# Kernel tuning notes

Measured on AMD Instinct MI355X. Metric: run time of the kernel, lower is better.

## Reference

```python
import jax, jax.numpy as jnp
import numpy as np

C = 256
NUM_HEADS = 4
GROUPS = 32  # max(1, 256//8), divides 256
EPS = 1e-5


def setup_inputs() -> dict:
    key = jax.random.key(0)
    ks = jax.random.split(key, 7)
    B, H, W = 4, 64, 64
    s = 0.02
    return {
        "x": jax.random.normal(ks[0], (B, C, H, W), dtype=jnp.float32),
        "norm_gamma": jnp.ones((C,), jnp.float32),
        "norm_beta": jnp.zeros((C,), jnp.float32),
        "qkv_w": jax.random.normal(ks[1], (3 * C, C), jnp.float32) * s,  # 1x1 conv kernel squeezed
        "qkv_b": jax.random.normal(ks[2], (3 * C,), jnp.float32) * s,
        "proj_w": jax.random.normal(ks[3], (C, C), jnp.float32) * s,
        "proj_b": jax.random.normal(ks[4], (C,), jnp.float32) * s,
    }


def reference(x, norm_gamma, norm_beta, qkv_w, qkv_b, proj_w, proj_b):
    B, Cc, H, W = x.shape
    hd = Cc // NUM_HEADS
    scale = hd ** -0.5

    # GroupNorm over (channels-per-group, H, W)
    xg = x.reshape(B, GROUPS, Cc // GROUPS, H, W)
    mu = xg.mean(axis=(2, 3, 4), keepdims=True)
    var = xg.var(axis=(2, 3, 4), keepdims=True)
    h = ((xg - mu) * jax.lax.rsqrt(var + EPS)).reshape(B, Cc, H, W)
    h = h * norm_gamma[:, None, None] + norm_beta[:, None, None]

    # 1x1 conv QKV: [B,3C,H,W]
    qkv = jnp.einsum('bchw,oc->bohw', h, qkv_w) + qkv_b[:, None, None]
    q, k, v = jnp.split(qkv, 3, axis=1)

    def heads(t):  # [B,C,H,W] -> [B,nh,HW,hd]
        return t.reshape(B, NUM_HEADS, hd, H * W).transpose(0, 1, 3, 2)

    q, k, v = heads(q), heads(k), heads(v)
    attn = jnp.einsum('bhnd,bhmd->bhnm', q, k) * scale  # [B,nh,HW,HW]
    attn = jax.nn.softmax(attn, axis=-1)
    out = jnp.einsum('bhnm,bhmd->bhnd', attn, v)  # [B,nh,HW,hd]
    out = out.transpose(0, 1, 3, 2).reshape(B, Cc, H, W)

    out = jnp.einsum('bchw,oc->bohw', out, proj_w) + proj_b[:, None, None]
    return x + out
```

## Files before the change

kernel.cpp:

```cpp
#include <hip/hip_runtime.h>
#include <hip/hip_bf16.h>
#include <stdint.h>

typedef unsigned short u16;
typedef __attribute__((ext_vector_type(8))) short bf16x8;
typedef __attribute__((ext_vector_type(4))) float f32x4;
typedef __attribute__((ext_vector_type(16))) float f32x16;

#define HW 4096
#define CC 256
#define QSCALE 0.18033688011112042f

__device__ __forceinline__ u16 f2bf(float f) {
    union { float f; uint32_t i; } v; v.f = f;
    uint32_t x = v.i;
    return (u16)((x + 0x7fffu + ((x >> 16) & 1u)) >> 16);
}

__device__ __forceinline__ float fast_exp2(float x) {
#if __has_builtin(__builtin_amdgcn_exp2f)
    return __builtin_amdgcn_exp2f(x);
#else
    return exp2f(x);
#endif
}

__device__ __forceinline__ unsigned cvt_pk_bf16(float lo, float hi) {
    unsigned r;
    asm("v_cvt_pk_bf16_f32 %0, %1, %2" : "=v"(r) : "v"(lo), "v"(hi));
    return r;
}

__device__ __forceinline__ void plane_swap(unsigned& a, unsigned& b) {
#if __has_builtin(__builtin_amdgcn_permlane32_swap)
    auto r = __builtin_amdgcn_permlane32_swap(a, b, false, false);
    a = r[0]; b = r[1];
#else
    unsigned ax = __shfl_xor((int)a, 32);
    unsigned bx = __shfl_xor((int)b, 32);
    bool hi = (threadIdx.x & 32) != 0;
    unsigned na = hi ? bx : a;
    unsigned nb = hi ? b : ax;
    a = na; b = nb;
#endif
}

#define MFMA16(a, b, c) __builtin_amdgcn_mfma_f32_16x16x32_bf16(a, b, c, 0, 0, 0)
#define MFMA32(a, b, c) __builtin_amdgcn_mfma_f32_32x32x16_bf16(a, b, c, 0, 0, 0)

__global__ void k_wsc(const float* __restrict__ qkv_w, const float* __restrict__ proj_w,
                      const float* __restrict__ x,
                      u16* __restrict__ wqkv, u16* __restrict__ wproj, float* __restrict__ stats) {
    int bid = blockIdx.x;
    if (bid < 128) {
        int bg = bid;
        const float4* p = reinterpret_cast<const float4*>(x + (size_t)bg * 8 * HW);
        float s = 0.f, ss = 0.f;
        for (int i = 0; i < 32; ++i) {
            float4 v = p[threadIdx.x + i * 256];
            s += v.x + v.y + v.z + v.w;
            ss += v.x * v.x + v.y * v.y + v.z * v.z + v.w * v.w;
        }
        __shared__ float rs[256], rss[256];
        rs[threadIdx.x] = s; rss[threadIdx.x] = ss;
        __syncthreads();
        for (int off = 128; off > 0; off >>= 1) {
            if (threadIdx.x < off) { rs[threadIdx.x] += rs[threadIdx.x + off]; rss[threadIdx.x] += rss[threadIdx.x + off]; }
            __syncthreads();
        }
        if (threadIdx.x == 0) {
            float mu = rs[0] * (1.f / 32768.f);
            float var = rss[0] * (1.f / 32768.f) - mu * mu;
            stats[bg * 2] = mu;
            stats[bg * 2 + 1] = rsqrtf(var + 1e-5f);
        }
    } else {
        int i = (bid - 128) * 256 + threadIdx.x;
        if (i < 768 * 256) {
            int o = i >> 8;
            float sc = (o < 256) ? QSCALE : 1.0f;
            wqkv[i] = f2bf(qkv_w[i] * sc);
        }
        int j = i - 768 * 256;
        if (j >= 0 && j < 256 * 256) wproj[j] = f2bf(proj_w[j]);
    }
}

__global__ __launch_bounds__(256) void k_gnt(const float* __restrict__ x, const float* __restrict__ stats,
                                             const float* __restrict__ gamma, const float* __restrict__ beta,
                                             u16* __restrict__ h_t) {
    int bid = blockIdx.x;
    int b = bid >> 8;
    int cb = (bid >> 6) & 3;
    int nb = bid & 63;
    int t = threadIdx.x;
    int cl = t >> 2;
    int ch = t & 3;
    int c = cb * 64 + cl;
    int g = c >> 3;
    float mu = stats[(b * 32 + g) * 2];
    float rsg = stats[(b * 32 + g) * 2 + 1];
    float ga = gamma[c], be = beta[c];
    __shared__ float T[64][66];
    const float4* p = reinterpret_cast<const float4*>(x + ((size_t)(b * CC + c)) * HW + nb * 64 + ch * 16);
    for (int j = 0; j < 4; ++j) {
        float4 v = p[j];
        int nbase = ch * 16 + j * 4;
        T[nbase + 0][cl] = (v.x - mu) * rsg * ga + be;
        T[nbase + 1][cl] = (v.y - mu) * rsg * ga + be;
        T[nbase + 2][cl] = (v.z - mu) * rsg * ga + be;
        T[nbase + 3][cl] = (v.w - mu) * rsg * ga + be;
    }
    __syncthreads();
    int nl = t >> 2;
    union { u16 u[16]; uint4 q[2]; } pk;
    for (int j = 0; j < 16; ++j) pk.u[j] = f2bf(T[nl][ch * 16 + j]);
    u16* dst = h_t + ((size_t)b * HW + nb * 64 + nl) * CC + cb * 64 + ch * 16;
    *reinterpret_cast<uint4*>(dst) = pk.q[0];
    *reinterpret_cast<uint4*>(dst + 8) = pk.q[1];
}

__global__ __launch_bounds__(256) void k_qkv(const u16* __restrict__ wqkv, const u16* __restrict__ h_t,
                                             const float* __restrict__ qkv_b,
                                             u16* __restrict__ qk_t, u16* __restrict__ v_o) {
    int bid = blockIdx.x;
    int b = bid / 192;
    int rem = bid % 192;
    int om = rem >> 5;
    int nb = rem & 31;
    int o0 = om * 128, n0 = nb * 128;
    int t = threadIdx.x;
    int wid = t >> 6, lane = t & 63;
    int wm = wid >> 1, wn = wid & 1;
    int l15 = lane & 15, lg = lane >> 4;

    __shared__ u16 sA[128 * 40], sB[128 * 40];
    f32x4 acc[4][4];
    for (int i = 0; i < 4; ++i) for (int j = 0; j < 4; ++j) acc[i][j] = (f32x4)0.f;

    const u16* gA = wqkv + (size_t)o0 * 256;
    const u16* gB = h_t + ((size_t)b * HW + n0) * CC;
    int row = t >> 1, half = t & 1;

    for (int kt = 0; kt < 8; ++kt) {
        __syncthreads();
        {
            const uint4* pa = reinterpret_cast<const uint4*>(gA + (size_t)row * 256 + kt * 32 + half * 16);
            uint4 a0 = pa[0], a1 = pa[1];
            const uint4* pb = reinterpret_cast<const uint4*>(gB + (size_t)row * 256 + kt * 32 + half * 16);
            uint4 b0 = pb[0], b1 = pb[1];
            *reinterpret_cast<uint4*>(&sA[row * 40 + half * 16]) = a0;
            *reinterpret_cast<uint4*>(&sA[row * 40 + half * 16 + 8]) = a1;
            *reinterpret_cast<uint4*>(&sB[row * 40 + half * 16]) = b0;
            *reinterpret_cast<uint4*>(&sB[row * 40 + half * 16 + 8]) = b1;
        }
        __syncthreads();
        bf16x8 af[4], bfr[4];
        for (int mt = 0; mt < 4; ++mt)
            af[mt] = *reinterpret_cast<const bf16x8*>(&sA[(wm * 64 + mt * 16 + l15) * 40 + lg * 8]);
        for (int nt = 0; nt < 4; ++nt)
            bfr[nt] = *reinterpret_cast<const bf16x8*>(&sB[(wn * 64 + nt * 16 + l15) * 40 + lg * 8]);
        for (int mt = 0; mt < 4; ++mt)
            for (int nt = 0; nt < 4; ++nt)
                acc[mt][nt] = MFMA16(af[mt], bfr[nt], acc[mt][nt]);
    }

    if (o0 < 512) {
        for (int mt = 0; mt < 4; ++mt) {
            int ob = o0 + wm * 64 + mt * 16 + lg * 4;
            float bias[4];
            for (int r = 0; r < 4; ++r) {
                int o = ob + r;
                bias[r] = qkv_b[o] * (o < 256 ? QSCALE : 1.0f);
            }
            for (int nt = 0; nt < 4; ++nt) {
                int n = n0 + wn * 64 + nt * 16 + l15;
                union { u16 u[4]; uint2 q; } pk;
                for (int r = 0; r < 4; ++r) pk.u[r] = f2bf(acc[mt][nt][r] + bias[r]);
                *reinterpret_cast<uint2*>(qk_t + ((size_t)b * HW + n) * 512 + ob) = pk.q;
            }
        }
    } else {
        for (int mt = 0; mt < 4; ++mt) {
            int ob = o0 + wm * 64 + mt * 16 + lg * 4;
            for (int nt = 0; nt < 4; ++nt) {
                int n = n0 + wn * 64 + nt * 16 + l15;
                for (int r = 0; r < 4; ++r) {
                    int o = ob + r;
                    float bias = qkv_b[o];
                    v_o[((size_t)b * 256 + (o - 512)) * HW + n] = f2bf(acc[mt][nt][r] + bias);
                }
            }
        }
    }
}

__global__ __launch_bounds__(512, 4) void k_attn(const u16* __restrict__ qk_t, const u16* __restrict__ v_o,
                                                 u16* __restrict__ ao_t) {
    int bid = blockIdx.x;
    int qb = bid & 31, head = (bid >> 5) & 3, b = bid >> 7;
    int n0 = qb * 128;
    int t = threadIdx.x;
    int kg = t >> 8;
    int wq = (t >> 6) & 3;
    int lane = t & 63, l31 = lane & 31, h = lane >> 5;

    __shared__ u16 lds[2 * 2 * 2 * 64 * 72];

    const u16* qbase = qk_t + ((size_t)b * HW + n0 + wq * 32 + l31) * 512 + head * 64 + h * 8;
    bf16x8 qf[4];
#pragma unroll
    for (int cs = 0; cs < 4; ++cs) qf[cs] = *reinterpret_cast<const bf16x8*>(qbase + cs * 16);

    const u16* gK = qk_t + (size_t)b * HW * 512 + 256 + head * 64;
    const u16* gV = v_o + ((size_t)b * 256 + head * 64) * (size_t)HW;

    int tIn = t & 255;
    int srow = tIn >> 3, sch = tIn & 7;
    const u16* pk0 = gK + (size_t)(kg * 2048 + srow) * 512 + sch * 8;
    const u16* pk1 = pk0 + 32 * 512;
    const u16* pv0 = gV + (size_t)srow * HW + kg * 2048 + sch * 8;
    const u16* pv1 = pv0 + 32 * HW;
    uint4 rk0 = *reinterpret_cast<const uint4*>(pk0);
    uint4 rk1 = *reinterpret_cast<const uint4*>(pk1);
    uint4 rv0 = *reinterpret_cast<const uint4*>(pv0);
    uint4 rv1 = *reinterpret_cast<const uint4*>(pv1);

    f32x16 o0 = (f32x16)0.f, o1 = (f32x16)0.f;
    float l_run = 0.f;
    u16* gb = lds + kg * 18432;

    for (int ti = 0; ti < 32; ++ti) {
        u16* bK = gb + (ti & 1) * 9216;
        u16* bV = bK + 4608;
        *reinterpret_cast<uint4*>(bK + srow * 72 + sch * 8) = rk0;
        *reinterpret_cast<uint4*>(bK + (srow + 32) * 72 + sch * 8) = rk1;
        *reinterpret_cast<uint4*>(bV + srow * 72 + sch * 8) = rv0;
        *reinterpret_cast<uint4*>(bV + (srow + 32) * 72 + sch * 8) = rv1;
        if (ti < 31) {
            pk0 += 64 * 512; pk1 += 64 * 512; pv0 += 64; pv1 += 64;
            rk0 = *reinterpret_cast<const uint4*>(pk0);
            rk1 = *reinterpret_cast<const uint4*>(pk1);
            rv0 = *reinterpret_cast<const uint4*>(pv0);
            rv1 = *reinterpret_cast<const uint4*>(pv1);
        }
        __syncthreads();

        f32x16 s0 = (f32x16)0.f, s1 = (f32x16)0.f;
#pragma unroll
        for (int cs = 0; cs < 4; ++cs) {
            bf16x8 k0 = *reinterpret_cast<const bf16x8*>(bK + l31 * 72 + cs * 16 + h * 8);
            bf16x8 k1 = *reinterpret_cast<const bf16x8*>(bK + (l31 + 32) * 72 + cs * 16 + h * 8);
            s0 = MFMA32(k0, qf[cs], s0);
            s1 = MFMA32(k1, qf[cs], s1);
        }

        float ps = 0.f;
#pragma unroll
        for (int i = 0; i < 16; ++i) { float e = fast_exp2(s0[i]); s0[i] = e; ps += e; }
#pragma unroll
        for (int i = 0; i < 16; ++i) { float e = fast_exp2(s1[i]); s1[i] = e; ps += e; }
        l_run += ps;

        unsigned dws[2][8];
#pragma unroll
        for (int a = 0; a < 4; ++a) {
            dws[0][2 * a]     = cvt_pk_bf16(s0[4 * a],     s0[4 * a + 1]);
            dws[0][2 * a + 1] = cvt_pk_bf16(s0[4 * a + 2], s0[4 * a + 3]);
            dws[1][2 * a]     = cvt_pk_bf16(s1[4 * a],     s1[4 * a + 1]);
            dws[1][2 * a + 1] = cvt_pk_bf16(s1[4 * a + 2], s1[4 * a + 3]);
        }
        bf16x8 pf[4];
#pragma unroll
        for (int ks = 0; ks < 4; ++ks) {
            int kt = ks >> 1, sf = ks & 1;
            unsigned A0 = dws[kt][4 * sf + 0], B0 = dws[kt][4 * sf + 2];
            unsigned A1 = dws[kt][4 * sf + 1], B1 = dws[kt][4 * sf + 3];
            plane_swap(A0, B0);
            plane_swap(A1, B1);
            union { unsigned d[4]; bf16x8 v; } u;
            u.d[0] = A0; u.d[1] = A1; u.d[2] = B0; u.d[3] = B1;
            pf[ks] = u.v;
        }

#pragma unroll
        for (int ks = 0; ks < 4; ++ks) {
            bf16x8 v0 = *reinterpret_cast<const bf16x8*>(bV + l31 * 72 + ks * 16 + h * 8);
            bf16x8 v1 = *reinterpret_cast<const bf16x8*>(bV + (l31 + 32) * 72 + ks * 16 + h * 8);
            o0 = MFMA32(v0, pf[ks], o0);
            o1 = MFMA32(v1, pf[ks], o1);
        }
    }

    l_run += __shfl_xor(l_run, 32);

    float* Of = (float*)lds;
    float* Lf = (float*)lds + 8192;
    u16* E = lds + 18432;

    __syncthreads();
    if (kg == 1) {
#pragma unroll
        for (int i = 0; i < 16; ++i) {
            Of[wq * 2048 + i * 64 + lane] = o0[i];
            Of[wq * 2048 + (16 + i) * 64 + lane] = o1[i];
        }
        Lf[wq * 64 + lane] = l_run;
    }
    __syncthreads();
    if (kg == 0) {
#pragma unroll
        for (int i = 0; i < 16; ++i) {
            o0[i] += Of[wq * 2048 + i * 64 + lane];
            o1[i] += Of[wq * 2048 + (16 + i) * 64 + lane];
        }
        l_run += Lf[wq * 64 + lane];
        float inv = 1.0f / l_run;
        int qrow = wq * 32 + l31;
#pragma unroll
        for (int r = 0; r < 16; ++r) {
            int d = (r & 3) + 8 * (r >> 2) + 4 * h;
            E[qrow * 72 + d]      = f2bf(o0[r] * inv);
            E[qrow * 72 + 32 + d] = f2bf(o1[r] * inv);
        }
    }
    __syncthreads();
#pragma unroll
    for (int i = 0; i < 2; ++i) {
        int item = i * 512 + t;
        int row = item >> 3, cb = item & 7;
        uint4 w = *reinterpret_cast<const uint4*>(E + row * 72 + cb * 8);
        *reinterpret_cast<uint4*>(ao_t + ((size_t)b * HW + n0 + row) * 256 + head * 64 + cb * 8) = w;
    }
}

__global__ __launch_bounds__(256) void k_proj(const u16* __restrict__ wproj, const u16* __restrict__ ao_t,
                                              const float* __restrict__ proj_b, const float* __restrict__ x,
                                              float* __restrict__ out) {
    int bid = blockIdx.x;
    int b = bid >> 6;
    int om = (bid >> 5) & 1;
    int nb = bid & 31;
    int o0 = om * 128, n0 = nb * 128;
    int t = threadIdx.x;
    int wid = t >> 6, lane = t & 63;
    int wm = wid >> 1, wn = wid & 1;
    int l15 = lane & 15, lg = lane >> 4;

    __shared__ u16 sA[128 * 40], sB[128 * 40];
    f32x4 acc[4][4];
    for (int i = 0; i < 4; ++i) for (int j = 0; j < 4; ++j) acc[i][j] = (f32x4)0.f;

    const u16* gA = wproj + (size_t)o0 * 256;
    const u16* gB = ao_t + ((size_t)b * HW + n0) * CC;
    int row = t >> 1, half = t & 1;

    for (int kt = 0; kt < 8; ++kt) {
        __syncthreads();
        {
            const uint4* pa = reinterpret_cast<const uint4*>(gA + (size_t)row * 256 + kt * 32 + half * 16);
            uint4 a0 = pa[0], a1 = pa[1];
            const uint4* pb = reinterpret_cast<const uint4*>(gB + (size_t)row * 256 + kt * 32 + half * 16);
            uint4 b0 = pb[0], b1 = pb[1];
            *reinterpret_cast<uint4*>(&sA[row * 40 + half * 16]) = a0;
            *reinterpret_cast<uint4*>(&sA[row * 40 + half * 16 + 8]) = a1;
            *reinterpret_cast<uint4*>(&sB[row * 40 + half * 16]) = b0;
            *reinterpret_cast<uint4*>(&sB[row * 40 + half * 16 + 8]) = b1;
        }
        __syncthreads();
        bf16x8 af[4], bfr[4];
        for (int mt = 0; mt < 4; ++mt)
            af[mt] = *reinterpret_cast<const bf16x8*>(&sA[(wm * 64 + mt * 16 + l15) * 40 + lg * 8]);
        for (int nt = 0; nt < 4; ++nt)
            bfr[nt] = *reinterpret_cast<const bf16x8*>(&sB[(wn * 64 + nt * 16 + l15) * 40 + lg * 8]);
        for (int mt = 0; mt < 4; ++mt)
            for (int nt = 0; nt < 4; ++nt)
                acc[mt][nt] = MFMA16(af[mt], bfr[nt], acc[mt][nt]);
    }

    for (int mt = 0; mt < 4; ++mt) {
        int ob = o0 + wm * 64 + mt * 16 + lg * 4;
        for (int nt = 0; nt < 4; ++nt) {
            int n = n0 + wn * 64 + nt * 16 + l15;
            for (int r = 0; r < 4; ++r) {
                int o = ob + r;
                size_t idx = ((size_t)(b * CC + o)) * HW + n;
                out[idx] = acc[mt][nt][r] + proj_b[o] + x[idx];
            }
        }
    }
}

extern "C" void kernel_launch(void* const* d_in, const int* in_sizes, int n_in,
                              void* d_out, int out_size, void* d_ws, size_t ws_size,
                              hipStream_t stream) {
    const float* x      = (const float*)d_in[0];
    const float* gamma  = (const float*)d_in[1];
    const float* beta   = (const float*)d_in[2];
    const float* qkv_w  = (const float*)d_in[3];
    const float* qkv_b  = (const float*)d_in[4];
    const float* proj_w = (const float*)d_in[5];
    const float* proj_b = (const float*)d_in[6];
    float* out = (float*)d_out;
    char* ws = (char*)d_ws;

    float* stats = (float*)ws;
    u16* wqkv  = (u16*)(ws + 4096);
    u16* wproj = (u16*)(ws + 4096 + 393216);
    u16* h_t   = (u16*)(ws + 1048576);
    u16* qk_t  = (u16*)(ws + 1048576 + 8388608);
    u16* v_o   = (u16*)(ws + 1048576 + 8388608 + 16777216);
    u16* ao_t  = (u16*)(ws + 1048576 + 8388608 + 16777216 + 8388608);

    k_wsc<<<dim3(1152), dim3(256), 0, stream>>>(qkv_w, proj_w, x, wqkv, wproj, stats);
    k_gnt<<<dim3(1024), dim3(256), 0, stream>>>(x, stats, gamma, beta, h_t);
    k_qkv<<<dim3(768), dim3(256), 0, stream>>>(wqkv, h_t, qkv_b, qk_t, v_o);
    k_attn<<<dim3(512), dim3(512), 0, stream>>>(qk_t, v_o, ao_t);
    k_proj<<<dim3(256), dim3(256), 0, stream>>>(wproj, ao_t, proj_b, x, out);
}
```

Before: 131.9 us.

## Load V fragments directly from global and halve attention block size

The attention kernel now uses 256-thread blocks covering 64 queries each (1024 blocks) instead of 512-thread blocks with 128 queries. V is no longer staged through LDS: each lane reads its MFMA operand fragments straight from global memory, interleaved with the QK/exp work, and only K goes through a smaller double-buffered LDS tile. The aim is to cut LDS traffic and footprint and to raise occupancy. The cost is uncoalesced, strided global reads of V and twice as many total K/V loads across blocks.

```diff
diff --git a/kernel.cpp b/kernel.cpp
--- a/kernel.cpp
+++ b/kernel.cpp
@@ -195,17 +195,18 @@
     }
 }
 
-__global__ __launch_bounds__(512, 4) void k_attn(const u16* __restrict__ qk_t, const u16* __restrict__ v_o,
+__global__ __launch_bounds__(256, 4) void k_attn(const u16* __restrict__ qk_t, const u16* __restrict__ v_o,
                                                  u16* __restrict__ ao_t) {
     int bid = blockIdx.x;
-    int qb = bid & 31, head = (bid >> 5) & 3, b = bid >> 7;
-    int n0 = qb * 128;
+    int qb = bid & 63, head = (bid >> 6) & 3, b = bid >> 8;
+    int n0 = qb * 64;
     int t = threadIdx.x;
-    int kg = t >> 8;
-    int wq = (t >> 6) & 3;
+    int wid = t >> 6;
+    int kg = wid >> 1;
+    int wq = wid & 1;
     int lane = t & 63, l31 = lane & 31, h = lane >> 5;
 
-    __shared__ u16 lds[2 * 2 * 2 * 64 * 72];
+    __shared__ u16 lds[2 * 2 * 64 * 72];
 
     const u16* qbase = qk_t + ((size_t)b * HW + n0 + wq * 32 + l31) * 512 + head * 64 + h * 8;
     bf16x8 qf[4];
@@ -213,38 +214,41 @@
     for (int cs = 0; cs < 4; ++cs) qf[cs] = *reinterpret_cast<const bf16x8*>(qbase + cs * 16);
 
     const u16* gK = qk_t + (size_t)b * HW * 512 + 256 + head * 64;
-    const u16* gV = v_o + ((size_t)b * 256 + head * 64) * (size_t)HW;
-
-    int tIn = t & 255;
-    int srow = tIn >> 3, sch = tIn & 7;
-    const u16* pk0 = gK + (size_t)(kg * 2048 + srow) * 512 + sch * 8;
-    const u16* pk1 = pk0 + 32 * 512;
-    const u16* pv0 = gV + (size_t)srow * HW + kg * 2048 + sch * 8;
-    const u16* pv1 = pv0 + 32 * HW;
-    uint4 rk0 = *reinterpret_cast<const uint4*>(pk0);
-    uint4 rk1 = *reinterpret_cast<const uint4*>(pk1);
-    uint4 rv0 = *reinterpret_cast<const uint4*>(pv0);
-    uint4 rv1 = *reinterpret_cast<const uint4*>(pv1);
+    const u16* gVr0 = v_o + ((size_t)(b * 256 + head * 64 + l31)) * HW + kg * 2048;
+    const u16* gVr1 = gVr0 + 32 * (size_t)HW;
+
+    int tIn = t & 127;
+    int srow = tIn >> 1, chunk = tIn & 1;
+    const u16* pK = gK + (size_t)(kg * 2048 + srow) * 512 + chunk * 32;
+    uint4 ka = *reinterpret_cast<const uint4*>(pK);
+    uint4 kb = *reinterpret_cast<const uint4*>(pK + 8);
+    uint4 kc = *reinterpret_cast<const uint4*>(pK + 16);
+    uint4 kd = *reinterpret_cast<const uint4*>(pK + 24);
 
     f32x16 o0 = (f32x16)0.f, o1 = (f32x16)0.f;
     float l_run = 0.f;
-    u16* gb = lds + kg * 18432;
 
     for (int ti = 0; ti < 32; ++ti) {
-        u16* bK = gb + (ti & 1) * 9216;
-        u16* bV = bK + 4608;
-        *reinterpret_cast<uint4*>(bK + srow * 72 + sch * 8) = rk0;
-        *reinterpret_cast<uint4*>(bK + (srow + 32) * 72 + sch * 8) = rk1;
-        *reinterpret_cast<uint4*>(bV + srow * 72 + sch * 8) = rv0;
-        *reinterpret_cast<uint4*>(bV + (srow + 32) * 72 + sch * 8) = rv1;
+        u16* bK = lds + (kg * 2 + (ti & 1)) * 4608;
+        u16* wr = bK + srow * 72 + chunk * 32;
+        *reinterpret_cast<uint4*>(wr) = ka;
+        *reinterpret_cast<uint4*>(wr + 8) = kb;
+        *reinterpret_cast<uint4*>(wr + 16) = kc;
+        *reinterpret_cast<uint4*>(wr + 24) = kd;
         if (ti < 31) {
-            pk0 += 64 * 512; pk1 += 64 * 512; pv0 += 64; pv1 += 64;
-            rk0 = *reinterpret_cast<const uint4*>(pk0);
-            rk1 = *reinterpret_cast<const uint4*>(pk1);
-            rv0 = *reinterpret_cast<const uint4*>(pv0);
-            rv1 = *reinterpret_cast<const uint4*>(pv1);
-        }
-        __syncthreads();
+            pK += 64 * 512;
+            ka = *reinterpret_cast<const uint4*>(pK);
+            kb = *reinterpret_cast<const uint4*>(pK + 8);
+            kc = *reinterpret_cast<const uint4*>(pK + 16);
+            kd = *reinterpret_cast<const uint4*>(pK + 24);
+        }
+        __syncthreads();
+
+        int koff = ti * 64 + h * 8;
+        bf16x8 vfA[4];
+#pragma unroll
+        for (int ks = 0; ks < 4; ++ks)
+            vfA[ks] = *reinterpret_cast<const bf16x8*>(gVr0 + koff + ks * 16);
 
         f32x16 s0 = (f32x16)0.f, s1 = (f32x16)0.f;
 #pragma unroll
@@ -261,6 +265,11 @@
 #pragma unroll
         for (int i = 0; i < 16; ++i) { float e = fast_exp2(s1[i]); s1[i] = e; ps += e; }
         l_run += ps;
+
+        bf16x8 vfB[4];
+#pragma unroll
+        for (int ks = 0; ks < 4; ++ks)
+            vfB[ks] = *reinterpret_cast<const bf16x8*>(gVr1 + koff + ks * 16);
 
         unsigned dws[2][8];
 #pragma unroll
@@ -284,19 +293,16 @@
         }
 
 #pragma unroll
-        for (int ks = 0; ks < 4; ++ks) {
-            bf16x8 v0 = *reinterpret_cast<const bf16x8*>(bV + l31 * 72 + ks * 16 + h * 8);
-            bf16x8 v1 = *reinterpret_cast<const bf16x8*>(bV + (l31 + 32) * 72 + ks * 16 + h * 8);
-            o0 = MFMA32(v0, pf[ks], o0);
-            o1 = MFMA32(v1, pf[ks], o1);
-        }
+        for (int ks = 0; ks < 4; ++ks) o0 = MFMA32(vfA[ks], pf[ks], o0);
+#pragma unroll
+        for (int ks = 0; ks < 4; ++ks) o1 = MFMA32(vfB[ks], pf[ks], o1);
     }
 
     l_run += __shfl_xor(l_run, 32);
 
     float* Of = (float*)lds;
-    float* Lf = (float*)lds + 8192;
-    u16* E = lds + 18432;
+    float* Lf = (float*)lds + 4096;
+    u16* E = lds + 8704;
 
     __syncthreads();
     if (kg == 1) {
@@ -327,7 +333,7 @@
     __syncthreads();
 #pragma unroll
     for (int i = 0; i < 2; ++i) {
-        int item = i * 512 + t;
+        int item = i * 256 + t;
         int row = item >> 3, cb = item & 7;
         uint4 w = *reinterpret_cast<const uint4*>(E + row * 72 + cb * 8);
         *reinterpret_cast<uint4*>(ao_t + ((size_t)b * HW + n0 + row) * 256 + head * 64 + cb * 8) = w;
@@ -415,6 +421,6 @@
     k_wsc<<<dim3(1152), dim3(256), 0, stream>>>(qkv_w, proj_w, x, wqkv, wproj, stats);
     k_gnt<<<dim3(1024), dim3(256), 0, stream>>>(x, stats, gamma, beta, h_t);
     k_qkv<<<dim3(768), dim3(256), 0, stream>>>(wqkv, h_t, qkv_b, qk_t, v_o);
-    k_attn<<<dim3(512), dim3(512), 0, stream>>>(qk_t, v_o, ao_t);
+    k_attn<<<dim3(1024), dim3(256), 0, stream>>>(qk_t, v_o, ao_t);
     k_proj<<<dim3(256), dim3(256), 0, stream>>>(wproj, ao_t, proj_b, x, out);
 }
```

New measurement: 201.9 us. 1.53x slower.

## Give each attention wave two query tiles to reuse K/V LDS fragments

Applied to the files above, without the earlier changes.

Cuts the attention block from 8 to 4 waves, and each wave now handles 64 query rows (two 32-row tiles) instead of 32. Each K and V fragment read from LDS then feeds twice as many MFMAs, which halves LDS read traffic per unit of work. Global-to-LDS staging is reorganised so each thread loads wider row segments for K or V across both key halves. The cost is higher register pressure (four accumulator sets plus four score sets per wave), with launch bounds lowered to 256 threads and 2 blocks, which may reduce occupancy and latency hiding.

```diff
diff --git a/kernel.cpp b/kernel.cpp
--- a/kernel.cpp
+++ b/kernel.cpp
@@ -195,139 +195,202 @@
     }
 }
 
-__global__ __launch_bounds__(512, 4) void k_attn(const u16* __restrict__ qk_t, const u16* __restrict__ v_o,
+__global__ __launch_bounds__(256, 2) void k_attn(const u16* __restrict__ qk_t, const u16* __restrict__ v_o,
                                                  u16* __restrict__ ao_t) {
     int bid = blockIdx.x;
     int qb = bid & 31, head = (bid >> 5) & 3, b = bid >> 7;
     int n0 = qb * 128;
     int t = threadIdx.x;
-    int kg = t >> 8;
-    int wq = (t >> 6) & 3;
+    int wid = t >> 6;
+    int kg = wid >> 1;
+    int st = wid & 1;
     int lane = t & 63, l31 = lane & 31, h = lane >> 5;
 
     __shared__ u16 lds[2 * 2 * 2 * 64 * 72];
 
-    const u16* qbase = qk_t + ((size_t)b * HW + n0 + wq * 32 + l31) * 512 + head * 64 + h * 8;
-    bf16x8 qf[4];
-#pragma unroll
-    for (int cs = 0; cs < 4; ++cs) qf[cs] = *reinterpret_cast<const bf16x8*>(qbase + cs * 16);
+    const u16* qbase = qk_t + ((size_t)b * HW + n0 + st * 64 + l31) * 512 + head * 64 + h * 8;
+    bf16x8 qf0[4], qf1[4];
+#pragma unroll
+    for (int cs = 0; cs < 4; ++cs) {
+        qf0[cs] = *reinterpret_cast<const bf16x8*>(qbase + cs * 16);
+        qf1[cs] = *reinterpret_cast<const bf16x8*>(qbase + 32 * 512 + cs * 16);
+    }
 
     const u16* gK = qk_t + (size_t)b * HW * 512 + 256 + head * 64;
     const u16* gV = v_o + ((size_t)b * 256 + head * 64) * (size_t)HW;
 
-    int tIn = t & 255;
-    int srow = tIn >> 3, sch = tIn & 7;
-    const u16* pk0 = gK + (size_t)(kg * 2048 + srow) * 512 + sch * 8;
-    const u16* pk1 = pk0 + 32 * 512;
-    const u16* pv0 = gV + (size_t)srow * HW + kg * 2048 + sch * 8;
-    const u16* pv1 = pv0 + 32 * HW;
-    uint4 rk0 = *reinterpret_cast<const uint4*>(pk0);
-    uint4 rk1 = *reinterpret_cast<const uint4*>(pk1);
-    uint4 rv0 = *reinterpret_cast<const uint4*>(pv0);
-    uint4 rv1 = *reinterpret_cast<const uint4*>(pv1);
-
-    f32x16 o0 = (f32x16)0.f, o1 = (f32x16)0.f;
-    float l_run = 0.f;
-    u16* gb = lds + kg * 18432;
+    int sop = t >> 7;
+    int tIn = t & 127;
+    int srow = tIn >> 1, shalf = tIn & 1;
+    const u16* pA; const u16* pB; int step;
+    if (sop == 0) { pA = gK + (size_t)srow * 512 + shalf * 32; pB = pA + (size_t)2048 * 512; step = 64 * 512; }
+    else          { pA = gV + (size_t)srow * HW + shalf * 32;  pB = pA + 2048;               step = 64; }
+    uint4 a0 = *reinterpret_cast<const uint4*>(pA);
+    uint4 a1 = *reinterpret_cast<const uint4*>(pA + 8);
+    uint4 a2 = *reinterpret_cast<const uint4*>(pA + 16);
+    uint4 a3 = *reinterpret_cast<const uint4*>(pA + 24);
+    uint4 b0 = *reinterpret_cast<const uint4*>(pB);
+    uint4 b1 = *reinterpret_cast<const uint4*>(pB + 8);
+    uint4 b2 = *reinterpret_cast<const uint4*>(pB + 16);
+    uint4 b3 = *reinterpret_cast<const uint4*>(pB + 24);
+
+    f32x16 o00 = (f32x16)0.f, o01 = (f32x16)0.f, o10 = (f32x16)0.f, o11 = (f32x16)0.f;
+    float l0 = 0.f, l1 = 0.f;
 
     for (int ti = 0; ti < 32; ++ti) {
-        u16* bK = gb + (ti & 1) * 9216;
-        u16* bV = bK + 4608;
-        *reinterpret_cast<uint4*>(bK + srow * 72 + sch * 8) = rk0;
-        *reinterpret_cast<uint4*>(bK + (srow + 32) * 72 + sch * 8) = rk1;
-        *reinterpret_cast<uint4*>(bV + srow * 72 + sch * 8) = rv0;
-        *reinterpret_cast<uint4*>(bV + (srow + 32) * 72 + sch * 8) = rv1;
+        int buf = ti & 1;
+        u16* w0 = lds + buf * 9216 + sop * 4608 + srow * 72 + shalf * 32;
+        u16* w1 = w0 + 18432;
+        *reinterpret_cast<uint4*>(w0) = a0;
+        *reinterpret_cast<uint4*>(w0 + 8) = a1;
+        *reinterpret_cast<uint4*>(w0 + 16) = a2;
+        *reinterpret_cast<uint4*>(w0 + 24) = a3;
+        *reinterpret_cast<uint4*>(w1) = b0;
+        *reinterpret_cast<uint4*>(w1 + 8) = b1;
+        *reinterpret_cast<uint4*>(w1 + 16) = b2;
+        *reinterpret_cast<uint4*>(w1 + 24) = b3;
         if (ti < 31) {
-            pk0 += 64 * 512; pk1 += 64 * 512; pv0 += 64; pv1 += 64;
-            rk0 = *reinterpret_cast<const uint4*>(pk0);
-            rk1 = *reinterpret_cast<const uint4*>(pk1);
-            rv0 = *reinterpret_cast<const uint4*>(pv0);
-            rv1 = *reinterpret_cast<const uint4*>(pv1);
-        }
-        __syncthreads();
-
-        f32x16 s0 = (f32x16)0.f, s1 = (f32x16)0.f;
+            pA += step; pB += step;
+            a0 = *reinterpret_cast<const uint4*>(pA);
+            a1 = *reinterpret_cast<const uint4*>(pA + 8);
+            a2 = *reinterpret_cast<const uint4*>(pA + 16);
+            a3 = *reinterpret_cast<const uint4*>(pA + 24);
+            b0 = *reinterpret_cast<const uint4*>(pB);
+            b1 = *reinterpret_cast<const uint4*>(pB + 8);
+            b2 = *reinterpret_cast<const uint4*>(pB + 16);
+            b3 = *reinterpret_cast<const uint4*>(pB + 24);
+        }
+        __syncthreads();
+
+        const u16* bK = lds + kg * 18432 + buf * 9216;
+        const u16* bV = bK + 4608;
+
+        f32x16 s00 = (f32x16)0.f, s01 = (f32x16)0.f, s10 = (f32x16)0.f, s11 = (f32x16)0.f;
 #pragma unroll
         for (int cs = 0; cs < 4; ++cs) {
             bf16x8 k0 = *reinterpret_cast<const bf16x8*>(bK + l31 * 72 + cs * 16 + h * 8);
             bf16x8 k1 = *reinterpret_cast<const bf16x8*>(bK + (l31 + 32) * 72 + cs * 16 + h * 8);
-            s0 = MFMA32(k0, qf[cs], s0);
-            s1 = MFMA32(k1, qf[cs], s1);
-        }
-
-        float ps = 0.f;
-#pragma unroll
-        for (int i = 0; i < 16; ++i) { float e = fast_exp2(s0[i]); s0[i] = e; ps += e; }
-#pragma unroll
-        for (int i = 0; i < 16; ++i) { float e = fast_exp2(s1[i]); s1[i] = e; ps += e; }
-        l_run += ps;
-
-        unsigned dws[2][8];
-#pragma unroll
-        for (int a = 0; a < 4; ++a) {
-            dws[0][2 * a]     = cvt_pk_bf16(s0[4 * a],     s0[4 * a + 1]);
-            dws[0][2 * a + 1] = cvt_pk_bf16(s0[4 * a + 2], s0[4 * a + 3]);
-            dws[1][2 * a]     = cvt_pk_bf16(s1[4 * a],     s1[4 * a + 1]);
-            dws[1][2 * a + 1] = cvt_pk_bf16(s1[4 * a + 2], s1[4 * a + 3]);
-        }
-        bf16x8 pf[4];
-#pragma unroll
-        for (int ks = 0; ks < 4; ++ks) {
-            int kt = ks >> 1, sf = ks & 1;
-            unsigned A0 = dws[kt][4 * sf + 0], B0 = dws[kt][4 * sf + 2];
-            unsigned A1 = dws[kt][4 * sf + 1], B1 = dws[kt][4 * sf + 3];
-            plane_swap(A0, B0);
-            plane_swap(A1, B1);
-            union { unsigned d[4]; bf16x8 v; } u;
-            u.d[0] = A0; u.d[1] = A1; u.d[2] = B0; u.d[3] = B1;
-            pf[ks] = u.v;
+            s00 = MFMA32(k0, qf0[cs], s00);
+            s01 = MFMA32(k0, qf1[cs], s01);
+            s10 = MFMA32(k1, qf0[cs], s10);
+            s11 = MFMA32(k1, qf1[cs], s11);
+        }
+
+        bf16x8 pf0[4], pf1[4];
+        {
+            float ps = 0.f;
+#pragma unroll
+            for (int i = 0; i < 16; ++i) { float e = fast_exp2(s00[i]); s00[i] = e; ps += e; }
+#pragma unroll
+            for (int i = 0; i < 16; ++i) { float e = fast_exp2(s10[i]); s10[i] = e; ps += e; }
+            l0 += ps;
+            unsigned dws[2][8];
+#pragma unroll
+            for (int a = 0; a < 4; ++a) {
+                dws[0][2 * a]     = cvt_pk_bf16(s00[4 * a],     s00[4 * a + 1]);
+                dws[0][2 * a + 1] = cvt_pk_bf16(s00[4 * a + 2], s00[4 * a + 3]);
+                dws[1][2 * a]     = cvt_pk_bf16(s10[4 * a],     s10[4 * a + 1]);
+                dws[1][2 * a + 1] = cvt_pk_bf16(s10[4 * a + 2], s10[4 * a + 3]);
+            }
+#pragma unroll
+            for (int ks = 0; ks < 4; ++ks) {
+                int kt = ks >> 1, sf = ks & 1;
+                unsigned A0 = dws[kt][4 * sf + 0], B0 = dws[kt][4 * sf + 2];
+                unsigned A1 = dws[kt][4 * sf + 1], B1 = dws[kt][4 * sf + 3];
+                plane_swap(A0, B0);
+                plane_swap(A1, B1);
+                union { unsigned d[4]; bf16x8 v; } u;
+                u.d[0] = A0; u.d[1] = A1; u.d[2] = B0; u.d[3] = B1;
+                pf0[ks] = u.v;
+            }
+        }
+        {
+            float ps = 0.f;
+#pragma unroll
+            for (int i = 0; i < 16; ++i) { float e = fast_exp2(s01[i]); s01[i] = e; ps += e; }
+#pragma unroll
+            for (int i = 0; i < 16; ++i) { float e = fast_exp2(s11[i]); s11[i] = e; ps += e; }
+            l1 += ps;
+            unsigned dws[2][8];
+#pragma unroll
+            for (int a = 0; a < 4; ++a) {
+                dws[0][2 * a]     = cvt_pk_bf16(s01[4 * a],     s01[4 * a + 1]);
+                dws[0][2 * a + 1] = cvt_pk_bf16(s01[4 * a + 2], s01[4 * a + 3]);
+                dws[1][2 * a]     = cvt_pk_bf16(s11[4 * a],     s11[4 * a + 1]);
+                dws[1][2 * a + 1] = cvt_pk_bf16(s11[4 * a + 2], s11[4 * a + 3]);
+            }
+#pragma unroll
+            for (int ks = 0; ks < 4; ++ks) {
+                int kt = ks >> 1, sf = ks & 1;
+                unsigned A0 = dws[kt][4 * sf + 0], B0 = dws[kt][4 * sf + 2];
+                unsigned A1 = dws[kt][4 * sf + 1], B1 = dws[kt][4 * sf + 3];
+                plane_swap(A0, B0);
+                plane_swap(A1, B1);
+                union { unsigned d[4]; bf16x8 v; } u;
+                u.d[0] = A0; u.d[1] = A1; u.d[2] = B0; u.d[3] = B1;
+                pf1[ks] = u.v;
+            }
         }
 
 #pragma unroll
         for (int ks = 0; ks < 4; ++ks) {
             bf16x8 v0 = *reinterpret_cast<const bf16x8*>(bV + l31 * 72 + ks * 16 + h * 8);
             bf16x8 v1 = *reinterpret_cast<const bf16x8*>(bV + (l31 + 32) * 72 + ks * 16 + h * 8);
-            o0 = MFMA32(v0, pf[ks], o0);
-            o1 = MFMA32(v1, pf[ks], o1);
-        }
-    }
-
-    l_run += __shfl_xor(l_run, 32);
+            o00 = MFMA32(v0, pf0[ks], o00);
+            o01 = MFMA32(v0, pf1[ks], o01);
+            o10 = MFMA32(v1, pf0[ks], o10);
+            o11 = MFMA32(v1, pf1[ks], o11);
+        }
+    }
+
+    l0 += __shfl_xor(l0, 32);
+    l1 += __shfl_xor(l1, 32);
 
     float* Of = (float*)lds;
-    float* Lf = (float*)lds + 8192;
-    u16* E = lds + 18432;
+    float* Lf = (float*)((char*)lds + 32768);
+    u16* E = (u16*)((char*)lds + 33792);
 
     __syncthreads();
     if (kg == 1) {
-#pragma unroll
-        for (int i = 0; i < 16; ++i) {
-            Of[wq * 2048 + i * 64 + lane] = o0[i];
-            Of[wq * 2048 + (16 + i) * 64 + lane] = o1[i];
-        }
-        Lf[wq * 64 + lane] = l_run;
+        float* dst = Of + st * 4096 + lane;
+#pragma unroll
+        for (int r = 0; r < 16; ++r) {
+            dst[r * 64]        = o00[r];
+            dst[(16 + r) * 64] = o01[r];
+            dst[(32 + r) * 64] = o10[r];
+            dst[(48 + r) * 64] = o11[r];
+        }
+        Lf[st * 128 + lane] = l0;
+        Lf[st * 128 + 64 + lane] = l1;
     }
     __syncthreads();
     if (kg == 0) {
-#pragma unroll
-        for (int i = 0; i < 16; ++i) {
-            o0[i] += Of[wq * 2048 + i * 64 + lane];
-            o1[i] += Of[wq * 2048 + (16 + i) * 64 + lane];
-        }
-        l_run += Lf[wq * 64 + lane];
-        float inv = 1.0f / l_run;
-        int qrow = wq * 32 + l31;
+        const float* src = Of + st * 4096 + lane;
+#pragma unroll
+        for (int r = 0; r < 16; ++r) {
+            o00[r] += src[r * 64];
+            o01[r] += src[(16 + r) * 64];
+            o10[r] += src[(32 + r) * 64];
+            o11[r] += src[(48 + r) * 64];
+        }
+        l0 += Lf[st * 128 + lane];
+        l1 += Lf[st * 128 + 64 + lane];
+        float i0 = 1.0f / l0, i1 = 1.0f / l1;
+        int row0 = st * 64 + l31;
+        int row1 = row0 + 32;
 #pragma unroll
         for (int r = 0; r < 16; ++r) {
             int d = (r & 3) + 8 * (r >> 2) + 4 * h;
-            E[qrow * 72 + d]      = f2bf(o0[r] * inv);
-            E[qrow * 72 + 32 + d] = f2bf(o1[r] * inv);
+            E[row0 * 72 + d]      = f2bf(o00[r] * i0);
+            E[row0 * 72 + 32 + d] = f2bf(o10[r] * i0);
+            E[row1 * 72 + d]      = f2bf(o01[r] * i1);
+            E[row1 * 72 + 32 + d] = f2bf(o11[r] * i1);
         }
     }
     __syncthreads();
 #pragma unroll
-    for (int i = 0; i < 2; ++i) {
-        int item = i * 512 + t;
+    for (int i = 0; i < 4; ++i) {
+        int item = i * 256 + t;
         int row = item >> 3, cb = item & 7;
         uint4 w = *reinterpret_cast<const uint4*>(E + row * 72 + cb * 8);
         *reinterpret_cast<uint4*>(ao_t + ((size_t)b * HW + n0 + row) * 256 + head * 64 + cb * 8) = w;
@@ -415,6 +478,6 @@
     k_wsc<<<dim3(1152), dim3(256), 0, stream>>>(qkv_w, proj_w, x, wqkv, wproj, stats);
     k_gnt<<<dim3(1024), dim3(256), 0, stream>>>(x, stats, gamma, beta, h_t);
     k_qkv<<<dim3(768), dim3(256), 0, stream>>>(wqkv, h_t, qkv_b, qk_t, v_o);
-    k_attn<<<dim3(512), dim3(512), 0, stream>>>(qk_t, v_o, ao_t);
+    k_attn<<<dim3(512), dim3(256), 0, stream>>>(qk_t, v_o, ao_t);
     k_proj<<<dim3(256), dim3(256), 0, stream>>>(wproj, ao_t, proj_b, x, out);
 }
```

Result: no change. 130.7 us (-0.9%).

## Drop split-KV in attention kernel, use 256-thread blocks with block swizzle

Applied to the files above, without the earlier changes.

The attention kernel no longer splits the key range across two 256-thread groups per block. Each block now has 4 waves that loop over all 64 key tiles, which removes the cross-group LDS reduction and halves LDS use. Tile staging is changed so half the threads load K and half load V, 64 bytes each. A block-index swizzle also spreads consecutive blocks across batches and heads. In exchange the serial loop per wave is twice as long and there are half as many waves in flight per block.

```diff
diff --git a/kernel.cpp b/kernel.cpp
--- a/kernel.cpp
+++ b/kernel.cpp
@@ -195,17 +195,17 @@
     }
 }
 
-__global__ __launch_bounds__(512, 4) void k_attn(const u16* __restrict__ qk_t, const u16* __restrict__ v_o,
+__global__ __launch_bounds__(256, 4) void k_attn(const u16* __restrict__ qk_t, const u16* __restrict__ v_o,
                                                  u16* __restrict__ ao_t) {
     int bid = blockIdx.x;
-    int qb = bid & 31, head = (bid >> 5) & 3, b = bid >> 7;
+    int swz = (bid & 7) * 64 + (bid >> 3);
+    int qb = swz & 31, head = (swz >> 5) & 3, b = swz >> 7;
     int n0 = qb * 128;
     int t = threadIdx.x;
-    int kg = t >> 8;
-    int wq = (t >> 6) & 3;
+    int wq = t >> 6;
     int lane = t & 63, l31 = lane & 31, h = lane >> 5;
 
-    __shared__ u16 lds[2 * 2 * 2 * 64 * 72];
+    __shared__ u16 lds[2 * 2 * 64 * 72];
 
     const u16* qbase = qk_t + ((size_t)b * HW + n0 + wq * 32 + l31) * 512 + head * 64 + h * 8;
     bf16x8 qf[4];
@@ -215,36 +215,39 @@
     const u16* gK = qk_t + (size_t)b * HW * 512 + 256 + head * 64;
     const u16* gV = v_o + ((size_t)b * 256 + head * 64) * (size_t)HW;
 
-    int tIn = t & 255;
-    int srow = tIn >> 3, sch = tIn & 7;
-    const u16* pk0 = gK + (size_t)(kg * 2048 + srow) * 512 + sch * 8;
-    const u16* pk1 = pk0 + 32 * 512;
-    const u16* pv0 = gV + (size_t)srow * HW + kg * 2048 + sch * 8;
-    const u16* pv1 = pv0 + 32 * HW;
-    uint4 rk0 = *reinterpret_cast<const uint4*>(pk0);
-    uint4 rk1 = *reinterpret_cast<const uint4*>(pk1);
-    uint4 rv0 = *reinterpret_cast<const uint4*>(pv0);
-    uint4 rv1 = *reinterpret_cast<const uint4*>(pv1);
+    int sop = t >> 7;
+    int tIn = t & 127;
+    int srow = tIn >> 1, shalf = tIn & 1;
+    const u16* pS;
+    long step;
+    if (sop == 0) { pS = gK + (size_t)srow * 512 + shalf * 32; step = 64 * 512; }
+    else          { pS = gV + (size_t)srow * HW + shalf * 32;  step = 64; }
+    uint4 a0 = *reinterpret_cast<const uint4*>(pS);
+    uint4 a1 = *reinterpret_cast<const uint4*>(pS + 8);
+    uint4 a2 = *reinterpret_cast<const uint4*>(pS + 16);
+    uint4 a3 = *reinterpret_cast<const uint4*>(pS + 24);
 
     f32x16 o0 = (f32x16)0.f, o1 = (f32x16)0.f;
     float l_run = 0.f;
-    u16* gb = lds + kg * 18432;
-
-    for (int ti = 0; ti < 32; ++ti) {
-        u16* bK = gb + (ti & 1) * 9216;
-        u16* bV = bK + 4608;
-        *reinterpret_cast<uint4*>(bK + srow * 72 + sch * 8) = rk0;
-        *reinterpret_cast<uint4*>(bK + (srow + 32) * 72 + sch * 8) = rk1;
-        *reinterpret_cast<uint4*>(bV + srow * 72 + sch * 8) = rv0;
-        *reinterpret_cast<uint4*>(bV + (srow + 32) * 72 + sch * 8) = rv1;
-        if (ti < 31) {
-            pk0 += 64 * 512; pk1 += 64 * 512; pv0 += 64; pv1 += 64;
-            rk0 = *reinterpret_cast<const uint4*>(pk0);
-            rk1 = *reinterpret_cast<const uint4*>(pk1);
-            rv0 = *reinterpret_cast<const uint4*>(pv0);
-            rv1 = *reinterpret_cast<const uint4*>(pv1);
-        }
-        __syncthreads();
+
+    for (int ti = 0; ti < 64; ++ti) {
+        int buf = ti & 1;
+        u16* w = lds + buf * 9216 + sop * 4608 + srow * 72 + shalf * 32;
+        *reinterpret_cast<uint4*>(w) = a0;
+        *reinterpret_cast<uint4*>(w + 8) = a1;
+        *reinterpret_cast<uint4*>(w + 16) = a2;
+        *reinterpret_cast<uint4*>(w + 24) = a3;
+        if (ti < 63) {
+            pS += step;
+            a0 = *reinterpret_cast<const uint4*>(pS);
+            a1 = *reinterpret_cast<const uint4*>(pS + 8);
+            a2 = *reinterpret_cast<const uint4*>(pS + 16);
+            a3 = *reinterpret_cast<const uint4*>(pS + 24);
+        }
+        __syncthreads();
+
+        const u16* bK = lds + buf * 9216;
+        const u16* bV = bK + 4608;
 
         f32x16 s0 = (f32x16)0.f, s1 = (f32x16)0.f;
 #pragma unroll
@@ -293,41 +296,20 @@
     }
 
     l_run += __shfl_xor(l_run, 32);
-
-    float* Of = (float*)lds;
-    float* Lf = (float*)lds + 8192;
-    u16* E = lds + 18432;
-
+    float inv = 1.0f / l_run;
+
+    u16* E = lds;
+    int qrow = wq * 32 + l31;
+#pragma unroll
+    for (int r = 0; r < 16; ++r) {
+        int d = (r & 3) + 8 * (r >> 2) + 4 * h;
+        E[qrow * 72 + d]      = f2bf(o0[r] * inv);
+        E[qrow * 72 + 32 + d] = f2bf(o1[r] * inv);
+    }
     __syncthreads();
-    if (kg == 1) {
-#pragma unroll
-        for (int i = 0; i < 16; ++i) {
-            Of[wq * 2048 + i * 64 + lane] = o0[i];
-            Of[wq * 2048 + (16 + i) * 64 + lane] = o1[i];
-        }
-        Lf[wq * 64 + lane] = l_run;
-    }
-    __syncthreads();
-    if (kg == 0) {
-#pragma unroll
-        for (int i = 0; i < 16; ++i) {
-            o0[i] += Of[wq * 2048 + i * 64 + lane];
-            o1[i] += Of[wq * 2048 + (16 + i) * 64 + lane];
-        }
-        l_run += Lf[wq * 64 + lane];
-        float inv = 1.0f / l_run;
-        int qrow = wq * 32 + l31;
-#pragma unroll
-        for (int r = 0; r < 16; ++r) {
-            int d = (r & 3) + 8 * (r >> 2) + 4 * h;
-            E[qrow * 72 + d]      = f2bf(o0[r] * inv);
-            E[qrow * 72 + 32 + d] = f2bf(o1[r] * inv);
-        }
-    }
-    __syncthreads();
-#pragma unroll
-    for (int i = 0; i < 2; ++i) {
-        int item = i * 512 + t;
+#pragma unroll
+    for (int i = 0; i < 4; ++i) {
+        int item = i * 256 + t;
         int row = item >> 3, cb = item & 7;
         uint4 w = *reinterpret_cast<const uint4*>(E + row * 72 + cb * 8);
         *reinterpret_cast<uint4*>(ao_t + ((size_t)b * HW + n0 + row) * 256 + head * 64 + cb * 8) = w;
@@ -415,6 +397,6 @@
     k_wsc<<<dim3(1152), dim3(256), 0, stream>>>(qkv_w, proj_w, x, wqkv, wproj, stats);
     k_gnt<<<dim3(1024), dim3(256), 0, stream>>>(x, stats, gamma, beta, h_t);
     k_qkv<<<dim3(768), dim3(256), 0, stream>>>(wqkv, h_t, qkv_b, qk_t, v_o);
-    k_attn<<<dim3(512), dim3(512), 0, stream>>>(qk_t, v_o, ao_t);
+    k_attn<<<dim3(512), dim3(256), 0, stream>>>(qk_t, v_o, ao_t);
     k_proj<<<dim3(256), dim3(256), 0, stream>>>(wproj, ao_t, proj_b, x, out);
 }
```

Result: no change. 132.4 us (+0.4%).
